# Performance work log

Measured on AMD Instinct MI355X. Metric: run time of the kernel, lower is better.

The kernel has to match this reference:

```python
import jax, jax.numpy as jnp
import numpy as np

H = 16  # hidden_size


def lstm_layer(x_seq, w_ih, w_hh, b_ih, b_hh):
    # x_seq: [B, T, Din]; PyTorch gate order i, f, g, o
    B = x_seq.shape[0]
    Hh = w_hh.shape[1]
    b = b_ih + b_hh

    def step(carry, x_t):
        h, c = carry
        g = x_t @ w_ih.T + h @ w_hh.T + b  # [B, 4H]
        i, f, gg, o = jnp.split(g, 4, axis=-1)
        i = jax.nn.sigmoid(i)
        f = jax.nn.sigmoid(f)
        gg = jnp.tanh(gg)
        o = jax.nn.sigmoid(o)
        c = f * c + i * gg
        h = o * jnp.tanh(c)
        return (h, c), h

    init = (jnp.zeros((B, Hh), x_seq.dtype), jnp.zeros((B, Hh), x_seq.dtype))
    (h_n, c_n), hs = jax.lax.scan(step, init, jnp.swapaxes(x_seq, 0, 1))
    return jnp.swapaxes(hs, 0, 1), h_n


def setup_inputs() -> dict:
    key = jax.random.key(0)
    ks = jax.random.split(key, 16)
    B, T, Din = 8192, 256, 1
    x = jax.random.normal(ks[0], (B, T, Din), dtype=jnp.float32)
    lin_in_w = jax.random.normal(ks[1], (H, Din), dtype=jnp.float32) * np.sqrt(2.0 / Din)
    lin_in_b = jnp.zeros((H,), dtype=jnp.float32)
    w_ih0 = jax.random.normal(ks[2], (4 * H, H), dtype=jnp.float32) * np.sqrt(2.0 / H)
    w_hh0 = jax.random.normal(ks[3], (4 * H, H), dtype=jnp.float32) * (1.0 / np.sqrt(H))
    b_ih0 = jnp.zeros((4 * H,), dtype=jnp.float32)
    b_hh0 = jnp.zeros((4 * H,), dtype=jnp.float32)
    w_ih1 = jax.random.normal(ks[4], (4 * H, H), dtype=jnp.float32) * np.sqrt(2.0 / H)
    w_hh1 = jax.random.normal(ks[5], (4 * H, H), dtype=jnp.float32) * (1.0 / np.sqrt(H))
    b_ih1 = jnp.zeros((4 * H,), dtype=jnp.float32)
    b_hh1 = jnp.zeros((4 * H,), dtype=jnp.float32)
    fc_h_w = jax.random.normal(ks[6], (H // 2, H), dtype=jnp.float32) * np.sqrt(2.0 / H)
    fc_h_b = jnp.zeros((H // 2,), dtype=jnp.float32)
    fc_o_w = jax.random.normal(ks[7], (1, H // 2), dtype=jnp.float32) * np.sqrt(2.0 / (H // 2))
    fc_o_b = jnp.zeros((1,), dtype=jnp.float32)
    return {"x": x, "lin_in_w": lin_in_w, "lin_in_b": lin_in_b,
            "w_ih0": w_ih0, "w_hh0": w_hh0, "b_ih0": b_ih0, "b_hh0": b_hh0,
            "w_ih1": w_ih1, "w_hh1": w_hh1, "b_ih1": b_ih1, "b_hh1": b_hh1,
            "fc_h_w": fc_h_w, "fc_h_b": fc_h_b, "fc_o_w": fc_o_w, "fc_o_b": fc_o_b}


def reference(x, lin_in_w, lin_in_b, w_ih0, w_hh0, b_ih0, b_hh0,
              w_ih1, w_hh1, b_ih1, b_hh1, fc_h_w, fc_h_b, fc_o_w, fc_o_b):
    # linear_in + ReLU  -> [B, T, H]
    h = jax.nn.relu(x @ lin_in_w.T + lin_in_b)
    # 2-layer LSTM (eval mode: inter-layer dropout is identity)
    h, _ = lstm_layer(h, w_ih0, w_hh0, b_ih0, b_hh0)
    _, h_last = lstm_layer(h, w_ih1, w_hh1, b_ih1, b_hh1)  # h_n of top layer [B, H]
    z = jax.nn.relu(h_last @ fc_h_w.T + fc_h_b)  # dropout is identity in eval
    out = z @ fc_o_w.T + fc_o_b  # [B, 1]
    return out.squeeze(-1)
```

## Files before the change

kernel.cpp:

```cpp
#include <hip/hip_runtime.h>
#include <math.h>


#define L2E 1.4426950408889634f
#define EPB 8

typedef _Float16 f16x8 __attribute__((ext_vector_type(8)));
typedef float    f32x4 __attribute__((ext_vector_type(4)));
typedef int      i32x4 __attribute__((ext_vector_type(4)));

__device__ __forceinline__ float sigm(float v) {
    return __builtin_amdgcn_rcpf(1.0f + __builtin_amdgcn_exp2f(-L2E * v));
}

__device__ __forceinline__ unsigned pkh(float a, float b) {
    const _Float16 ha = (_Float16)a, hb = (_Float16)b;
    return (unsigned)__builtin_bit_cast(unsigned short, ha) |
           ((unsigned)__builtin_bit_cast(unsigned short, hb) << 16);
}
__device__ __forceinline__ float unpk(unsigned w, int hi) {
    const unsigned short s = (unsigned short)(hi ? (w >> 16) : (w & 0xffffu));
    return (float)__builtin_bit_cast(_Float16, s);
}
__device__ __forceinline__ f16x8 frag4(unsigned w0, unsigned w1,
                                       unsigned w2, unsigned w3) {
    i32x4 t = {(int)w0, (int)w1, (int)w2, (int)w3};
    return __builtin_bit_cast(f16x8, t);
}

#define GATES1(ACC, A, BIAS, BH)                                                      \
    _Pragma("unroll")                                                                 \
    for (int m = 0; m < 4; ++m) {                                                     \
        ACC[m] = BIAS[m];                                                             \
        ACC[m] = __builtin_amdgcn_mfma_f32_16x16x32_f16(A[m], BH, ACC[m], 0, 0, 0);   \
    }

#define COMBINE2(ACC, CA, CB, OWN)                                                    \
    do {                                                                              \
        const float aI0 = hi8 ? ACC[0][2] : ACC[0][0];                                \
        const float aI1 = hi8 ? ACC[0][3] : ACC[0][1];                                \
        const float aF0 = hi8 ? ACC[1][2] : ACC[1][0];                                \
        const float aF1 = hi8 ? ACC[1][3] : ACC[1][1];                                \
        const float aG0 = hi8 ? ACC[2][2] : ACC[2][0];                                \
        const float aG1 = hi8 ? ACC[2][3] : ACC[2][1];                                \
        const float aO0 = hi8 ? ACC[3][2] : ACC[3][0];                                \
        const float aO1 = hi8 ? ACC[3][3] : ACC[3][1];                                \
                                                                          \
        const float Ei0 = __builtin_amdgcn_exp2f(-L2E * aI0);                         \
        const float Ef0 = __builtin_amdgcn_exp2f(-L2E * aF0);                         \
        const float Eg0 = __builtin_amdgcn_exp2f(fmaxf(aG0, -40.0f) * (-2.0f * L2E)); \
        const float Eo0 = __builtin_amdgcn_exp2f(-L2E * aO0);                         \
        const float fp0 = 1.0f + Ef0;                                                 \
        const float P0  = (1.0f + Ei0) * (1.0f + Eg0);                                \
        const float N0  = fmaf(CA, P0, (1.0f - Eg0) * fp0);                           \
        CA = N0 * __builtin_amdgcn_rcpf(fp0 * P0);                                    \
        const float Ec0 = __builtin_amdgcn_exp2f(fmaxf(CA, -40.0f) * (-2.0f * L2E));  \
        const float h0_ = (1.0f - Ec0) *                                              \
            __builtin_amdgcn_rcpf((1.0f + Eo0) * (1.0f + Ec0));                       \
                                                                          \
        const float Ei1 = __builtin_amdgcn_exp2f(-L2E * aI1);                         \
        const float Ef1 = __builtin_amdgcn_exp2f(-L2E * aF1);                         \
        const float Eg1 = __builtin_amdgcn_exp2f(fmaxf(aG1, -40.0f) * (-2.0f * L2E)); \
        const float Eo1 = __builtin_amdgcn_exp2f(-L2E * aO1);                         \
        const float fp1 = 1.0f + Ef1;                                                 \
        const float P1  = (1.0f + Ei1) * (1.0f + Eg1);                                \
        const float N1  = fmaf(CB, P1, (1.0f - Eg1) * fp1);                           \
        CB = N1 * __builtin_amdgcn_rcpf(fp1 * P1);                                    \
        const float Ec1 = __builtin_amdgcn_exp2f(fmaxf(CB, -40.0f) * (-2.0f * L2E));  \
        const float h1_ = (1.0f - Ec1) *                                              \
            __builtin_amdgcn_rcpf((1.0f + Eo1) * (1.0f + Ec1));                       \
        OWN = pkh(h0_, h1_);                                                          \
    } while (0)

#define EXCH(OWN, W0, W1)                                                             \
    do {                                                                              \
        const unsigned oth_ = (unsigned)__shfl_xor((int)(OWN), 8, 64);                \
        W0 = hi8 ? oth_ : (OWN);                                                      \
        W1 = hi8 ? (OWN) : oth_;                                                      \
    } while (0)

__global__ __launch_bounds__(64) void lstm_dup(
    const float* __restrict__ x,
    const float* __restrict__ w_in, const float* __restrict__ b_in,
    const float* __restrict__ w_ih0, const float* __restrict__ w_hh0,
    const float* __restrict__ b_ih0, const float* __restrict__ b_hh0,
    const float* __restrict__ w_ih1, const float* __restrict__ w_hh1,
    const float* __restrict__ b_ih1, const float* __restrict__ b_hh1,
    const float* __restrict__ fc_h_w, const float* __restrict__ fc_h_b,
    const float* __restrict__ fc_o_w, const float* __restrict__ fc_o_b,
    float* __restrict__ out, int B, int T)
{
    const int lane = threadIdx.x;
    const int e    = lane & 15;
    const int g    = lane >> 4;
    const bool hi8 = (e >= 8);
    const int base = blockIdx.x * EPB;
    int rowe = base + (e & 7); if (rowe >= B) rowe = B - 1;

    __shared__ float htab[EPB][16];

    f16x8 a0[4], a1[4];
    f32x4 bias0[4], bias1[4];
    #pragma unroll
    for (int m = 0; m < 4; ++m) {
        const int r = 16 * m + e;
        #pragma unroll
        for (int i = 0; i < 8; ++i) {
            const float w0 = (i < 4) ? w_ih0[r * 16 + 4 * g + i]
                                     : w_hh0[r * 16 + 4 * g + (i - 4)];
            const float w1 = (i < 4) ? w_ih1[r * 16 + 4 * g + i]
                                     : w_hh1[r * 16 + 4 * g + (i - 4)];
            a0[m][i] = (_Float16)w0;
            a1[m][i] = (_Float16)w1;
        }
        const int rd = 16 * m + 4 * g;
        #pragma unroll
        for (int q = 0; q < 4; ++q) {
            bias0[m][q] = b_ih0[rd + q] + b_hh0[rd + q];
            bias1[m][q] = b_ih1[rd + q] + b_hh1[rd + q];
        }
    }
    float winq[4], binq[4];
    #pragma unroll
    for (int q = 0; q < 4; ++q) { winq[q] = w_in[4 * g + q]; binq[q] = b_in[4 * g + q]; }

    float c0A = 0.f, c0B = 0.f, c1A = 0.f, c1B = 0.f;
    unsigned h0w0, h0w1;
    unsigned h1w0 = 0u, h1w1 = 0u;
    unsigned h1own = 0u;

    const float* xrow = x + (size_t)rowe * T;

    {
        const float xv = xrow[0];
        const unsigned xw0 = pkh(fmaxf(fmaf(xv, winq[0], binq[0]), 0.0f),
                                 fmaxf(fmaf(xv, winq[1], binq[1]), 0.0f));
        const unsigned xw1 = pkh(fmaxf(fmaf(xv, winq[2], binq[2]), 0.0f),
                                 fmaxf(fmaf(xv, winq[3], binq[3]), 0.0f));
        const f16x8 Bh = frag4(xw0, xw1, 0u, 0u);
        f32x4 acc[4];
        GATES1(acc, a0, bias0, Bh);
        unsigned own;
        COMBINE2(acc, c0A, c0B, own);
        EXCH(own, h0w0, h0w1);
    }

    float xv1 = xrow[(T > 1) ? 1 : 0];

    for (int t = 0; t < T - 1; ++t) {
        const int tn = (t + 2 < T) ? (t + 2) : (T - 1);
        const float xn = xrow[tn];

        const unsigned xw0 = pkh(fmaxf(fmaf(xv1, winq[0], binq[0]), 0.0f),
                                 fmaxf(fmaf(xv1, winq[1], binq[1]), 0.0f));
        const unsigned xw1 = pkh(fmaxf(fmaf(xv1, winq[2], binq[2]), 0.0f),
                                 fmaxf(fmaf(xv1, winq[3], binq[3]), 0.0f));

        const f16x8 B0h = frag4(xw0, xw1, h0w0, h0w1);
        const f16x8 B1h = frag4(h0w0, h0w1, h1w0, h1w1);

        f32x4 acc0[4], acc1[4];
        GATES1(acc0, a0, bias0, B0h);
        GATES1(acc1, a1, bias1, B1h);

        unsigned own0, own1;
        COMBINE2(acc0, c0A, c0B, own0);
        COMBINE2(acc1, c1A, c1B, own1);

        EXCH(own0, h0w0, h0w1);
        EXCH(own1, h1w0, h1w1);
        h1own = own1;
        xv1 = xn;
    }

    {
        const f16x8 Bh = frag4(h0w0, h0w1, h1w0, h1w1);
        f32x4 acc[4];
        GATES1(acc, a1, bias1, Bh);
        unsigned own;
        COMBINE2(acc, c1A, c1B, own);
        EXCH(own, h1w0, h1w1);
        h1own = own;
        (void)h1own;
    }

    if (!hi8) {
        htab[e][4 * g + 0] = unpk(h1w0, 0);
        htab[e][4 * g + 1] = unpk(h1w0, 1);
        htab[e][4 * g + 2] = unpk(h1w1, 0);
        htab[e][4 * g + 3] = unpk(h1w1, 1);
    }
    __syncthreads();
    if (lane < EPB) {
        const int ee = lane;
        float hv[16];
        #pragma unroll
        for (int k = 0; k < 16; ++k) hv[k] = htab[ee][k];
        float z[8];
        #pragma unroll
        for (int p = 0; p < 8; ++p) {
            float acc = fc_h_b[p];
            #pragma unroll
            for (int k = 0; k < 16; ++k) acc = fmaf(fc_h_w[p * 16 + k], hv[k], acc);
            z[p] = fmaxf(acc, 0.0f);
        }
        float o = fc_o_b[0];
        #pragma unroll
        for (int p = 0; p < 8; ++p) o = fmaf(fc_o_w[p], z[p], o);
        if (base + ee < B) out[base + ee] = o;
    }
}

extern "C" void kernel_launch(void* const* d_in, const int* in_sizes, int n_in,
                              void* d_out, int out_size, void* d_ws, size_t ws_size,
                              hipStream_t stream) {
    const float* x      = (const float*)d_in[0];
    const float* w_in   = (const float*)d_in[1];
    const float* b_in   = (const float*)d_in[2];
    const float* w_ih0  = (const float*)d_in[3];
    const float* w_hh0  = (const float*)d_in[4];
    const float* b_ih0  = (const float*)d_in[5];
    const float* b_hh0  = (const float*)d_in[6];
    const float* w_ih1  = (const float*)d_in[7];
    const float* w_hh1  = (const float*)d_in[8];
    const float* b_ih1  = (const float*)d_in[9];
    const float* b_hh1  = (const float*)d_in[10];
    const float* fc_h_w = (const float*)d_in[11];
    const float* fc_h_b = (const float*)d_in[12];
    const float* fc_o_w = (const float*)d_in[13];
    const float* fc_o_b = (const float*)d_in[14];

    const int B = out_size;
    const int T = in_sizes[0] / (B > 0 ? B : 1);
    const int grid = (B + EPB - 1) / EPB;

    hipLaunchKernelGGL(lstm_dup, dim3(grid), dim3(64), 0, stream,
                       x, w_in, b_in, w_ih0, w_hh0, b_ih0, b_hh0,
                       w_ih1, w_hh1, b_ih1, b_hh1, fc_h_w, fc_h_b,
                       fc_o_w, fc_o_b, (float*)d_out, B, T);
}
```

Before: 122.4 us.

## Halve batch elements per wave so each lane computes one hidden unit

Each 64-lane block now handles 4 batch elements instead of 8. The MFMA columns are replicated four times, so each lane runs one LSTM cell's transcendental chain instead of two. The h exchange becomes a two-stage shuffle (xor 4, then xor 8) to rebuild the packed f16 fragment. This shortens the serial per-step activation work on the recurrence critical path. In exchange it doubles the grid size and the total MFMA work, and adds one shuffle per step.

```diff
diff --git a/kernel.cpp b/kernel.cpp
--- a/kernel.cpp
+++ b/kernel.cpp
@@ -3,20 +3,19 @@
 
 
 #define L2E 1.4426950408889634f
-#define EPB 8
+#define EPB 4
 
 typedef _Float16 f16x8 __attribute__((ext_vector_type(8)));
 typedef float    f32x4 __attribute__((ext_vector_type(4)));
 typedef int      i32x4 __attribute__((ext_vector_type(4)));
-
-__device__ __forceinline__ float sigm(float v) {
-    return __builtin_amdgcn_rcpf(1.0f + __builtin_amdgcn_exp2f(-L2E * v));
-}
 
 __device__ __forceinline__ unsigned pkh(float a, float b) {
     const _Float16 ha = (_Float16)a, hb = (_Float16)b;
     return (unsigned)__builtin_bit_cast(unsigned short, ha) |
            ((unsigned)__builtin_bit_cast(unsigned short, hb) << 16);
+}
+__device__ __forceinline__ unsigned h16(float a) {
+    return (unsigned)__builtin_bit_cast(unsigned short, (_Float16)a);
 }
 __device__ __forceinline__ float unpk(unsigned w, int hi) {
     const unsigned short s = (unsigned short)(hi ? (w >> 16) : (w & 0xffffu));
@@ -35,51 +34,37 @@
         ACC[m] = __builtin_amdgcn_mfma_f32_16x16x32_f16(A[m], BH, ACC[m], 0, 0, 0);   \
     }
 
-#define COMBINE2(ACC, CA, CB, OWN)                                                    \
+#define SEL4(V) (q1 ? (q0 ? (V)[3] : (V)[2]) : (q0 ? (V)[1] : (V)[0]))
+
+#define COMBINE1(ACC, CC, HB)                                                         \
     do {                                                                              \
-        const float aI0 = hi8 ? ACC[0][2] : ACC[0][0];                                \
-        const float aI1 = hi8 ? ACC[0][3] : ACC[0][1];                                \
-        const float aF0 = hi8 ? ACC[1][2] : ACC[1][0];                                \
-        const float aF1 = hi8 ? ACC[1][3] : ACC[1][1];                                \
-        const float aG0 = hi8 ? ACC[2][2] : ACC[2][0];                                \
-        const float aG1 = hi8 ? ACC[2][3] : ACC[2][1];                                \
-        const float aO0 = hi8 ? ACC[3][2] : ACC[3][0];                                \
-        const float aO1 = hi8 ? ACC[3][3] : ACC[3][1];                                \
-                                                                          \
-        const float Ei0 = __builtin_amdgcn_exp2f(-L2E * aI0);                         \
-        const float Ef0 = __builtin_amdgcn_exp2f(-L2E * aF0);                         \
-        const float Eg0 = __builtin_amdgcn_exp2f(fmaxf(aG0, -40.0f) * (-2.0f * L2E)); \
-        const float Eo0 = __builtin_amdgcn_exp2f(-L2E * aO0);                         \
-        const float fp0 = 1.0f + Ef0;                                                 \
-        const float P0  = (1.0f + Ei0) * (1.0f + Eg0);                                \
-        const float N0  = fmaf(CA, P0, (1.0f - Eg0) * fp0);                           \
-        CA = N0 * __builtin_amdgcn_rcpf(fp0 * P0);                                    \
-        const float Ec0 = __builtin_amdgcn_exp2f(fmaxf(CA, -40.0f) * (-2.0f * L2E));  \
-        const float h0_ = (1.0f - Ec0) *                                              \
-            __builtin_amdgcn_rcpf((1.0f + Eo0) * (1.0f + Ec0));                       \
-                                                                          \
-        const float Ei1 = __builtin_amdgcn_exp2f(-L2E * aI1);                         \
-        const float Ef1 = __builtin_amdgcn_exp2f(-L2E * aF1);                         \
-        const float Eg1 = __builtin_amdgcn_exp2f(fmaxf(aG1, -40.0f) * (-2.0f * L2E)); \
-        const float Eo1 = __builtin_amdgcn_exp2f(-L2E * aO1);                         \
-        const float fp1 = 1.0f + Ef1;                                                 \
-        const float P1  = (1.0f + Ei1) * (1.0f + Eg1);                                \
-        const float N1  = fmaf(CB, P1, (1.0f - Eg1) * fp1);                           \
-        CB = N1 * __builtin_amdgcn_rcpf(fp1 * P1);                                    \
-        const float Ec1 = __builtin_amdgcn_exp2f(fmaxf(CB, -40.0f) * (-2.0f * L2E));  \
-        const float h1_ = (1.0f - Ec1) *                                              \
-            __builtin_amdgcn_rcpf((1.0f + Eo1) * (1.0f + Ec1));                       \
-        OWN = pkh(h0_, h1_);                                                          \
+        const float aI_ = SEL4(ACC[0]);                                               \
+        const float aF_ = SEL4(ACC[1]);                                               \
+        const float aG_ = SEL4(ACC[2]);                                               \
+        const float aO_ = SEL4(ACC[3]);                                               \
+        const float Ei_ = __builtin_amdgcn_exp2f(-L2E * aI_);                         \
+        const float Ef_ = __builtin_amdgcn_exp2f(-L2E * aF_);                         \
+        const float Eg_ = __builtin_amdgcn_exp2f(fmaxf(aG_, -40.0f) * (-2.0f * L2E)); \
+        const float Eo_ = __builtin_amdgcn_exp2f(-L2E * aO_);                         \
+        const float fp_ = 1.0f + Ef_;                                                 \
+        const float P_  = (1.0f + Ei_) * (1.0f + Eg_);                                \
+        const float N_  = fmaf(CC, P_, (1.0f - Eg_) * fp_);                           \
+        CC = N_ * __builtin_amdgcn_rcpf(fp_ * P_);                                    \
+        const float Ec_ = __builtin_amdgcn_exp2f(fmaxf(CC, -40.0f) * (-2.0f * L2E));  \
+        HB = h16((1.0f - Ec_) *                                                       \
+                 __builtin_amdgcn_rcpf((1.0f + Eo_) * (1.0f + Ec_)));                 \
     } while (0)
 
-#define EXCH(OWN, W0, W1)                                                             \
+#define EXCH4(HB, W0, W1)                                                             \
     do {                                                                              \
-        const unsigned oth_ = (unsigned)__shfl_xor((int)(OWN), 8, 64);                \
-        W0 = hi8 ? oth_ : (OWN);                                                      \
-        W1 = hi8 ? (OWN) : oth_;                                                      \
+        const unsigned po_ = (unsigned)__shfl_xor((int)(HB), 4, 64);                  \
+        const unsigned pw_ = q0 ? (po_ | ((HB) << 16)) : ((HB) | (po_ << 16));        \
+        const unsigned ow_ = (unsigned)__shfl_xor((int)pw_, 8, 64);                   \
+        W0 = q1 ? ow_ : pw_;                                                          \
+        W1 = q1 ? pw_ : ow_;                                                          \
     } while (0)
 
-__global__ __launch_bounds__(64) void lstm_dup(
+__global__ __launch_bounds__(64) void lstm_dup4(
     const float* __restrict__ x,
     const float* __restrict__ w_in, const float* __restrict__ b_in,
     const float* __restrict__ w_ih0, const float* __restrict__ w_hh0,
@@ -93,9 +78,10 @@
     const int lane = threadIdx.x;
     const int e    = lane & 15;
     const int g    = lane >> 4;
-    const bool hi8 = (e >= 8);
+    const bool q0  = (e & 4) != 0;
+    const bool q1  = (e & 8) != 0;
     const int base = blockIdx.x * EPB;
-    int rowe = base + (e & 7); if (rowe >= B) rowe = B - 1;
+    int rowe = base + (e & 3); if (rowe >= B) rowe = B - 1;
 
     __shared__ float htab[EPB][16];
 
@@ -124,10 +110,9 @@
     #pragma unroll
     for (int q = 0; q < 4; ++q) { winq[q] = w_in[4 * g + q]; binq[q] = b_in[4 * g + q]; }
 
-    float c0A = 0.f, c0B = 0.f, c1A = 0.f, c1B = 0.f;
+    float c0 = 0.f, c1 = 0.f;
     unsigned h0w0, h0w1;
     unsigned h1w0 = 0u, h1w1 = 0u;
-    unsigned h1own = 0u;
 
     const float* xrow = x + (size_t)rowe * T;
 
@@ -140,9 +125,9 @@
         const f16x8 Bh = frag4(xw0, xw1, 0u, 0u);
         f32x4 acc[4];
         GATES1(acc, a0, bias0, Bh);
-        unsigned own;
-        COMBINE2(acc, c0A, c0B, own);
-        EXCH(own, h0w0, h0w1);
+        unsigned hb;
+        COMBINE1(acc, c0, hb);
+        EXCH4(hb, h0w0, h0w1);
     }
 
     float xv1 = xrow[(T > 1) ? 1 : 0];
@@ -163,13 +148,12 @@
         GATES1(acc0, a0, bias0, B0h);
         GATES1(acc1, a1, bias1, B1h);
 
-        unsigned own0, own1;
-        COMBINE2(acc0, c0A, c0B, own0);
-        COMBINE2(acc1, c1A, c1B, own1);
-
-        EXCH(own0, h0w0, h0w1);
-        EXCH(own1, h1w0, h1w1);
-        h1own = own1;
+        unsigned hb0, hb1;
+        COMBINE1(acc0, c0, hb0);
+        COMBINE1(acc1, c1, hb1);
+
+        EXCH4(hb0, h0w0, h0w1);
+        EXCH4(hb1, h1w0, h1w1);
         xv1 = xn;
     }
 
@@ -177,14 +161,12 @@
         const f16x8 Bh = frag4(h0w0, h0w1, h1w0, h1w1);
         f32x4 acc[4];
         GATES1(acc, a1, bias1, Bh);
-        unsigned own;
-        COMBINE2(acc, c1A, c1B, own);
-        EXCH(own, h1w0, h1w1);
-        h1own = own;
-        (void)h1own;
-    }
-
-    if (!hi8) {
+        unsigned hb;
+        COMBINE1(acc, c1, hb);
+        EXCH4(hb, h1w0, h1w1);
+    }
+
+    if (!q0 && !q1) {
         htab[e][4 * g + 0] = unpk(h1w0, 0);
         htab[e][4 * g + 1] = unpk(h1w0, 1);
         htab[e][4 * g + 2] = unpk(h1w1, 0);
@@ -234,7 +216,7 @@
     const int T = in_sizes[0] / (B > 0 ? B : 1);
     const int grid = (B + EPB - 1) / EPB;
 
-    hipLaunchKernelGGL(lstm_dup, dim3(grid), dim3(64), 0, stream,
+    hipLaunchKernelGGL(lstm_dup4, dim3(grid), dim3(64), 0, stream,
                        x, w_in, b_in, w_ih0, w_hh0, b_ih0, b_hh0,
                        w_ih1, w_hh1, b_ih1, b_hh1, fc_h_w, fc_h_b,
                        fc_o_w, fc_o_b, (float*)d_out, B, T);
```

After: 160.6 us. 1.31x slower.
